# Optimization experiments

Measured on AMD Instinct MI355X. Metric: run time of the kernel, lower is better.

The kernel has to match this reference:

```python
import jax, jax.numpy as jnp
import numpy as np
from jax import lax

VOCAB = 128
UNITS = 1024
B, T = 64, 128


def setup_inputs() -> dict:
    key = jax.random.key(0)
    ks = jax.random.split(key, 8)
    tokens = jax.random.randint(ks[0], (B, T), 0, VOCAB)
    emb_table = jax.random.normal(ks[1], (VOCAB, UNITS), dtype=jnp.float32) * 0.05
    def dir_params(k):
        k1, k2, k3 = jax.random.split(k, 3)
        W = jax.random.normal(k1, (UNITS, 3 * UNITS), dtype=jnp.float32) * 0.02
        U = jax.random.normal(k2, (UNITS, 3 * UNITS), dtype=jnp.float32) * 0.02
        b = jnp.zeros((2, 3 * UNITS), dtype=jnp.float32)  # [input_bias, recurrent_bias] (reset_after=True)
        return W, U, b
    Wf, Uf, bf = dir_params(ks[2])
    Wb, Ub, bb = dir_params(ks[3])
    return {"tokens": tokens, "emb_table": emb_table,
            "Wf": Wf, "Uf": Uf, "bf": bf,
            "Wb": Wb, "Ub": Ub, "bb": bb}


def _gru_dir(emb, mask, W, U, b):
    """Masked GRU (Keras semantics, reset_after=True, gate order z,r,h).
    emb: [B,T,U] float, mask: [B,T] bool. Returns [B,T,U]."""
    units = W.shape[0]
    # Precompute input projection for all timesteps (one big GEMM).
    xp = jnp.einsum('btu,uv->btv', emb, W) + b[0]          # [B,T,3U]
    xp_t = jnp.transpose(xp, (1, 0, 2))                     # [T,B,3U]
    m_t = jnp.transpose(mask, (1, 0))                       # [T,B]
    h0 = jnp.zeros((emb.shape[0], units), dtype=emb.dtype)
    out0 = jnp.zeros_like(h0)

    def step(carry, inp):
        h, prev_out = carry
        x_t, mt = inp
        rec = h @ U + b[1]                                  # [B,3U]
        xz, xr, xh = jnp.split(x_t, 3, axis=-1)
        rz, rr, rh = jnp.split(rec, 3, axis=-1)
        z = jax.nn.sigmoid(xz + rz)
        r = jax.nn.sigmoid(xr + rr)
        hh = jnp.tanh(xh + r * rh)
        h_new = z * h + (1.0 - z) * hh
        m = mt[:, None]
        out = jnp.where(m, h_new, prev_out)  # masked steps copy previous output
        h_next = jnp.where(m, h_new, h)      # masked steps carry state
        return (h_next, out), out

    _, outs = lax.scan(step, (h0, out0), (xp_t, m_t))       # [T,B,U]
    return jnp.transpose(outs, (1, 0, 2))


def reference(tokens, emb_table, Wf, Uf, bf, Wb, Ub, bb):
    mask = tokens != 0                                      # mask_zero=True
    emb = emb_table[tokens]                                 # [B,T,U]
    fwd = _gru_dir(emb, mask, Wf, Uf, bf)
    # backward direction: reverse time, run GRU, reverse output back
    bwd = _gru_dir(emb[:, ::-1, :], mask[:, ::-1], Wb, Ub, bb)[:, ::-1, :]
    return fwd + bwd                                        # merge_mode='sum'
```

## Files before the change

### kernel.cpp

```cpp
#include <hip/hip_runtime.h>
#include <hip/hip_cooperative_groups.h>

namespace cg = cooperative_groups;

#define NWG 256
#define NT  256
#define B_  64
#define T_  128
#define U_  1024
#define C3  3072
#define SMEM_BYTES ((24*1024 + 2*64*12) * 4)

__device__ __forceinline__ float sigm(float x){ return 1.f/(1.f+__expf(-x)); }
__device__ __forceinline__ float tanh_(float x){ return 1.f - 2.f/(1.f+__expf(2.f*x)); }

__global__ void __launch_bounds__(NT, 1)
enc_kernel(const int* __restrict__ tok,
           const float* __restrict__ emb,
           const float* __restrict__ Wf, const float* __restrict__ Uf, const float* __restrict__ bfp,
           const float* __restrict__ Wb, const float* __restrict__ Ub, const float* __restrict__ bbp,
           float* __restrict__ out, float* __restrict__ ws)
{
  extern __shared__ float sm[];
  float* Ul   = sm;
  float* recl = sm + 24*1024;

  const int tid = threadIdx.x, wg = blockIdx.x;
  const int u0 = wg*4;

  float* xpv  = ws;
  float* embT = ws + 6144*128;
  float* hg   = ws + 6144*128 + 1024*128;

  cg::grid_group grid = cg::this_grid();
  const int gtid = wg*NT + tid;

  for (int i = gtid; i < 2*1024*64; i += NWG*NT) hg[i] = 0.f;
  for (int i = gtid; i < 128*1024; i += NWG*NT)
    embT[(i & 1023)*128 + (i >> 10)] = emb[i];

  #pragma unroll
  for (int i = 0; i < 24; ++i) {
    int flat = tid + i*NT;
    int k = flat / 6, rem = flat % 6;
    int dd = rem / 3, g = rem % 3;
    const float* M = dd ? Wb : Wf;
    float4 v4 = *(const float4*)&M[k*C3 + g*U_ + u0];
    Ul[(dd*12 + 0 + g)*1024 + k] = v4.x;
    Ul[(dd*12 + 3 + g)*1024 + k] = v4.y;
    Ul[(dd*12 + 6 + g)*1024 + k] = v4.z;
    Ul[(dd*12 + 9 + g)*1024 + k] = v4.w;
  }
  grid.sync();

  const int lane = tid & 63, wv = tid >> 6;
  const int d = wv >> 1, uu = wv & 1;
  const int bq = lane & 15, kq = lane >> 4;
  const float* ulds = Ul + (d*12 + uu*6)*1024;

  auto dot6 = [&](const float* src, int rs, float* r) {
    float acc[6][4];
    #pragma unroll
    for (int j=0;j<6;++j){acc[j][0]=acc[j][1]=acc[j][2]=acc[j][3]=0.f;}
    for (int kit = 0; kit < 64; ++kit) {
      float4 uv[6];
      #pragma unroll
      for (int j=0;j<6;++j) uv[j] = *(const float4*)(ulds + j*1024 + kq*256 + kit*4);
      #pragma unroll
      for (int kk=0;kk<4;++kk) {
        float4 h4 = *(const float4*)(src + (kit*4+kk)*rs);
        #pragma unroll
        for (int j=0;j<6;++j) {
          float w = kk==0?uv[j].x : kk==1?uv[j].y : kk==2?uv[j].z : uv[j].w;
          acc[j][0] += h4.x*w; acc[j][1] += h4.y*w;
          acc[j][2] += h4.z*w; acc[j][3] += h4.w*w;
        }
      }
    }
    #pragma unroll
    for (int j=0;j<6;++j){
      #pragma unroll
      for (int bi=0;bi<4;++bi){
        float v = acc[j][bi];
        v += __shfl_xor(v, 16, 64);
        v += __shfl_xor(v, 32, 64);
        acc[j][bi] = v;
      }
      r[j] = kq==0?acc[j][0] : kq==1?acc[j][1] : kq==2?acc[j][2] : acc[j][3];
    }
  };

  {
    const float* bias_d = d ? bbp : bfp;
    for (int half = 0; half < 2; ++half) {
      float r[6];
      dot6(embT + (kq*256)*128 + half*64 + bq*4, 128, r);
      int v = half*64 + bq*4 + kq;
      #pragma unroll
      for (int j=0;j<6;++j){
        int ul = j/3, g = j%3;
        int cp = g*U_ + u0 + uu*2 + ul;
        xpv[(d*C3 + cp)*128 + v] = r[j] + bias_d[cp];
      }
    }
  }
  __syncthreads();
  #pragma unroll
  for (int i = 0; i < 24; ++i) {
    int flat = tid + i*NT;
    int k = flat / 6, rem = flat % 6;
    int dd = rem / 3, g = rem % 3;
    const float* M = dd ? Ub : Uf;
    float4 v4 = *(const float4*)&M[k*C3 + g*U_ + u0];
    Ul[(dd*12 + 0 + g)*1024 + k] = v4.x;
    Ul[(dd*12 + 3 + g)*1024 + k] = v4.y;
    Ul[(dd*12 + 6 + g)*1024 + k] = v4.z;
    Ul[(dd*12 + 9 + g)*1024 + k] = v4.w;
  }
  __syncthreads();

  for (int s = 0; s < T_; ++s) {
    const float* hc = hg + (s&1)*(2*1024*64);
    float*       hn = hg + ((s+1)&1)*(2*1024*64);

    float r[6];
    dot6(hc + (d*1024 + kq*256)*64 + bq*4, 64, r);
    const int b = bq*4 + kq;
    #pragma unroll
    for (int j=0;j<6;++j) recl[(d*64 + b)*12 + uu*6 + j] = r[j];
    __syncthreads();

    {
      const int gd = tid >> 7, guu = (tid >> 6) & 1, gb = tid & 63;
      const int t = gd ? (T_-1 - s) : s;
      const int tk = tok[gb*T_ + t];
      const bool msk = (tk != 0);
      const float* bias = gd ? bbp : bfp;
      float o[2];
      #pragma unroll
      for (int ul=0; ul<2; ++ul) {
        const int u = u0 + guu*2 + ul;
        const int rb = (gd*64+gb)*12 + guu*6 + ul*3;
        float rz = recl[rb+0] + bias[C3 + u];
        float rr = recl[rb+1] + bias[C3 + U_ + u];
        float rh = recl[rb+2] + bias[C3 + 2*U_ + u];
        float xz = xpv[(gd*C3 +          u)*128 + tk];
        float xr = xpv[(gd*C3 +   U_  +  u)*128 + tk];
        float xh = xpv[(gd*C3 + 2*U_  +  u)*128 + tk];
        float hold = hc[(gd*1024 + u)*64 + gb];
        float z  = sigm(xz + rz);
        float rg = sigm(xr + rr);
        float th = tanh_(xh + rg*rh);
        float hnew = z*hold + (1.f - z)*th;
        float hx = msk ? hnew : hold;
        hn[(gd*1024 + u)*64 + gb] = hx;
        o[ul] = hx;
      }
      float2* op = (float2*)(out + (gb*T_ + t)*U_ + u0 + guu*2);
      if (s < 64) { *op = make_float2(o[0], o[1]); }
      else        { float2 pv = *op; *op = make_float2(pv.x + o[0], pv.y + o[1]); }
    }
    grid.sync();
  }
}

extern "C" void kernel_launch(void* const* d_in, const int* in_sizes, int n_in,
                              void* d_out, int out_size, void* d_ws, size_t ws_size,
                              hipStream_t stream) {
  const int*   tok = (const int*)  d_in[0];
  const float* emb = (const float*)d_in[1];
  const float* Wf  = (const float*)d_in[2];
  const float* Uf  = (const float*)d_in[3];
  const float* bfp = (const float*)d_in[4];
  const float* Wb  = (const float*)d_in[5];
  const float* Ub  = (const float*)d_in[6];
  const float* bbp = (const float*)d_in[7];
  float* outp = (float*)d_out;
  float* wsp  = (float*)d_ws;

  static bool attr_done = false;
  (void)attr_done;
  hipFuncSetAttribute((const void*)enc_kernel,
                      hipFuncAttributeMaxDynamicSharedMemorySize, SMEM_BYTES);

  void* args[] = { (void*)&tok, (void*)&emb, (void*)&Wf, (void*)&Uf, (void*)&bfp,
                   (void*)&Wb, (void*)&Ub, (void*)&bbp, (void*)&outp, (void*)&wsp };
  hipLaunchCooperativeKernel((const void*)enc_kernel, dim3(NWG), dim3(NT),
                             args, SMEM_BYTES, stream);
}
```

Measured before the change: 7.229 ms.

## Double threads per workgroup with K-split dot products and padded LDS layout

```diff
diff --git a/kernel.cpp b/kernel.cpp
--- a/kernel.cpp
+++ b/kernel.cpp
@@ -4,17 +4,22 @@
 namespace cg = cooperative_groups;
 
 #define NWG 256
-#define NT  256
+#define NT  512
 #define B_  64
 #define T_  128
 #define U_  1024
 #define C3  3072
-#define SMEM_BYTES ((24*1024 + 2*64*12) * 4)
+
+#define COLSTRIDE 1088
+#define U_LDS_FLOATS (24*COLSTRIDE)
+#define P_OFF   U_LDS_FLOATS
+#define REC_OFF (P_OFF + 6144)
+#define SMEM_BYTES ((U_LDS_FLOATS + 6144 + 1536)*4)
 
 __device__ __forceinline__ float sigm(float x){ return 1.f/(1.f+__expf(-x)); }
 __device__ __forceinline__ float tanh_(float x){ return 1.f - 2.f/(1.f+__expf(2.f*x)); }
 
-__global__ void __launch_bounds__(NT, 1)
+__global__ void __launch_bounds__(NT, 2)
 enc_kernel(const int* __restrict__ tok,
            const float* __restrict__ emb,
            const float* __restrict__ Wf, const float* __restrict__ Uf, const float* __restrict__ bfp,
@@ -23,7 +28,8 @@
 {
   extern __shared__ float sm[];
   float* Ul   = sm;
-  float* recl = sm + 24*1024;
+  float* Pl   = sm + P_OFF;
+  float* recl = sm + REC_OFF;
 
   const int tid = threadIdx.x, wg = blockIdx.x;
   const int u0 = wg*4;
@@ -39,38 +45,43 @@
   for (int i = gtid; i < 128*1024; i += NWG*NT)
     embT[(i & 1023)*128 + (i >> 10)] = emb[i];
 
-  #pragma unroll
-  for (int i = 0; i < 24; ++i) {
-    int flat = tid + i*NT;
-    int k = flat / 6, rem = flat % 6;
-    int dd = rem / 3, g = rem % 3;
-    const float* M = dd ? Wb : Wf;
-    float4 v4 = *(const float4*)&M[k*C3 + g*U_ + u0];
-    Ul[(dd*12 + 0 + g)*1024 + k] = v4.x;
-    Ul[(dd*12 + 3 + g)*1024 + k] = v4.y;
-    Ul[(dd*12 + 6 + g)*1024 + k] = v4.z;
-    Ul[(dd*12 + 9 + g)*1024 + k] = v4.w;
-  }
+  auto loadMat = [&](const float* Mf_, const float* Mb_) {
+    #pragma unroll
+    for (int i = 0; i < 12; ++i) {
+      int flat = tid + i*NT;
+      int k = flat / 6, rem = flat % 6;
+      int dd = rem / 3, g = rem % 3;
+      const float* M = dd ? Mb_ : Mf_;
+      float4 v4 = *(const float4*)&M[k*C3 + g*U_ + u0];
+      int koff = (k >> 6)*68 + (k & 63);
+      Ul[(dd*12 + 0*3 + g)*COLSTRIDE + koff] = v4.x;
+      Ul[(dd*12 + 1*3 + g)*COLSTRIDE + koff] = v4.y;
+      Ul[(dd*12 + 2*3 + g)*COLSTRIDE + koff] = v4.z;
+      Ul[(dd*12 + 3*3 + g)*COLSTRIDE + koff] = v4.w;
+    }
+  };
+
+  loadMat(Wf, Wb);
   grid.sync();
 
   const int lane = tid & 63, wv = tid >> 6;
-  const int d = wv >> 1, uu = wv & 1;
+  const int d = wv >> 2, kh = wv & 3;
   const int bq = lane & 15, kq = lane >> 4;
-  const float* ulds = Ul + (d*12 + uu*6)*1024;
+  const float* ubase = Ul + (d*12)*COLSTRIDE + (kh*4 + kq)*68;
 
-  auto dot6 = [&](const float* src, int rs, float* r) {
-    float acc[6][4];
+  auto dot12 = [&](const float* src, int rs, float* r) {
+    float acc[12][4];
     #pragma unroll
-    for (int j=0;j<6;++j){acc[j][0]=acc[j][1]=acc[j][2]=acc[j][3]=0.f;}
-    for (int kit = 0; kit < 64; ++kit) {
-      float4 uv[6];
+    for (int j=0;j<12;++j){acc[j][0]=acc[j][1]=acc[j][2]=acc[j][3]=0.f;}
+    for (int kit = 0; kit < 16; ++kit) {
+      float4 uv[12];
       #pragma unroll
-      for (int j=0;j<6;++j) uv[j] = *(const float4*)(ulds + j*1024 + kq*256 + kit*4);
+      for (int j=0;j<12;++j) uv[j] = *(const float4*)(ubase + j*COLSTRIDE + kit*4);
       #pragma unroll
       for (int kk=0;kk<4;++kk) {
         float4 h4 = *(const float4*)(src + (kit*4+kk)*rs);
         #pragma unroll
-        for (int j=0;j<6;++j) {
+        for (int j=0;j<12;++j) {
           float w = kk==0?uv[j].x : kk==1?uv[j].y : kk==2?uv[j].z : uv[j].w;
           acc[j][0] += h4.x*w; acc[j][1] += h4.y*w;
           acc[j][2] += h4.z*w; acc[j][3] += h4.w*w;
@@ -78,7 +89,7 @@
       }
     }
     #pragma unroll
-    for (int j=0;j<6;++j){
+    for (int j=0;j<12;++j){
       #pragma unroll
       for (int bi=0;bi<4;++bi){
         float v = acc[j][bi];
@@ -90,75 +101,71 @@
     }
   };
 
-  {
-    const float* bias_d = d ? bbp : bfp;
-    for (int half = 0; half < 2; ++half) {
-      float r[6];
-      dot6(embT + (kq*256)*128 + half*64 + bq*4, 128, r);
-      int v = half*64 + bq*4 + kq;
-      #pragma unroll
-      for (int j=0;j<6;++j){
-        int ul = j/3, g = j%3;
-        int cp = g*U_ + u0 + uu*2 + ul;
-        xpv[(d*C3 + cp)*128 + v] = r[j] + bias_d[cp];
-      }
+  for (int half = 0; half < 2; ++half) {
+    float r[12];
+    dot12(embT + (kh*256 + kq*64)*128 + half*64 + bq*4, 128, r);
+    const int vv = bq*4 + kq;
+    #pragma unroll
+    for (int j=0;j<12;++j) Pl[(d*12+j)*256 + kh*64 + vv] = r[j];
+    __syncthreads();
+    for (int e = tid; e < 1536; e += NT) {
+      int dc = e >> 6, v = e & 63;
+      float s_ = Pl[dc*256 + v] + Pl[dc*256 + 64 + v] + Pl[dc*256 + 128 + v] + Pl[dc*256 + 192 + v];
+      int dd = dc / 12, c = dc % 12;
+      int ul = c / 3, g = c % 3;
+      int cp = g*U_ + u0 + ul;
+      const float* brow = dd ? bbp : bfp;
+      xpv[(dd*C3 + cp)*128 + half*64 + v] = s_ + brow[cp];
     }
+    __syncthreads();
   }
+
+  loadMat(Uf, Ub);
   __syncthreads();
-  #pragma unroll
-  for (int i = 0; i < 24; ++i) {
-    int flat = tid + i*NT;
-    int k = flat / 6, rem = flat % 6;
-    int dd = rem / 3, g = rem % 3;
-    const float* M = dd ? Ub : Uf;
-    float4 v4 = *(const float4*)&M[k*C3 + g*U_ + u0];
-    Ul[(dd*12 + 0 + g)*1024 + k] = v4.x;
-    Ul[(dd*12 + 3 + g)*1024 + k] = v4.y;
-    Ul[(dd*12 + 6 + g)*1024 + k] = v4.z;
-    Ul[(dd*12 + 9 + g)*1024 + k] = v4.w;
-  }
-  __syncthreads();
+
+  const int gd = tid >> 8, grm = tid & 255, gb = grm >> 2, gul = grm & 3;
+  const int gu = u0 + gul;
+  const float* brow1 = (gd ? bbp : bfp) + C3;
+  const float bz1 = brow1[gu], br1 = brow1[U_ + gu], bh1 = brow1[2*U_ + gu];
 
   for (int s = 0; s < T_; ++s) {
     const float* hc = hg + (s&1)*(2*1024*64);
     float*       hn = hg + ((s+1)&1)*(2*1024*64);
 
-    float r[6];
-    dot6(hc + (d*1024 + kq*256)*64 + bq*4, 64, r);
+    float r[12];
+    dot12(hc + (d*1024 + kh*256 + kq*64)*64 + bq*4, 64, r);
     const int b = bq*4 + kq;
     #pragma unroll
-    for (int j=0;j<6;++j) recl[(d*64 + b)*12 + uu*6 + j] = r[j];
+    for (int j=0;j<12;++j) Pl[(d*12+j)*256 + kh*64 + b] = r[j];
+    __syncthreads();
+
+    #pragma unroll
+    for (int e = tid, it = 0; it < 3; ++it, e += NT) {
+      int dc = e >> 6, v = e & 63;
+      recl[e] = Pl[dc*256 + v] + Pl[dc*256 + 64 + v] + Pl[dc*256 + 128 + v] + Pl[dc*256 + 192 + v];
+    }
     __syncthreads();
 
     {
-      const int gd = tid >> 7, guu = (tid >> 6) & 1, gb = tid & 63;
       const int t = gd ? (T_-1 - s) : s;
       const int tk = tok[gb*T_ + t];
       const bool msk = (tk != 0);
-      const float* bias = gd ? bbp : bfp;
-      float o[2];
-      #pragma unroll
-      for (int ul=0; ul<2; ++ul) {
-        const int u = u0 + guu*2 + ul;
-        const int rb = (gd*64+gb)*12 + guu*6 + ul*3;
-        float rz = recl[rb+0] + bias[C3 + u];
-        float rr = recl[rb+1] + bias[C3 + U_ + u];
-        float rh = recl[rb+2] + bias[C3 + 2*U_ + u];
-        float xz = xpv[(gd*C3 +          u)*128 + tk];
-        float xr = xpv[(gd*C3 +   U_  +  u)*128 + tk];
-        float xh = xpv[(gd*C3 + 2*U_  +  u)*128 + tk];
-        float hold = hc[(gd*1024 + u)*64 + gb];
-        float z  = sigm(xz + rz);
-        float rg = sigm(xr + rr);
-        float th = tanh_(xh + rg*rh);
-        float hnew = z*hold + (1.f - z)*th;
-        float hx = msk ? hnew : hold;
-        hn[(gd*1024 + u)*64 + gb] = hx;
-        o[ul] = hx;
-      }
-      float2* op = (float2*)(out + (gb*T_ + t)*U_ + u0 + guu*2);
-      if (s < 64) { *op = make_float2(o[0], o[1]); }
-      else        { float2 pv = *op; *op = make_float2(pv.x + o[0], pv.y + o[1]); }
+      const int rb = (gd*12 + gul*3)*64 + gb;
+      float rz = recl[rb]        + bz1;
+      float rr = recl[rb + 64]   + br1;
+      float rh = recl[rb + 128]  + bh1;
+      float xz = xpv[(gd*C3 +          gu)*128 + tk];
+      float xr = xpv[(gd*C3 +   U_  +  gu)*128 + tk];
+      float xh = xpv[(gd*C3 + 2*U_  +  gu)*128 + tk];
+      float hold = hc[(gd*1024 + gu)*64 + gb];
+      float z  = sigm(xz + rz);
+      float rg = sigm(xr + rr);
+      float th = tanh_(xh + rg*rh);
+      float hnew = z*hold + (1.f - z)*th;
+      float hx = msk ? hnew : hold;
+      hn[(gd*1024 + gu)*64 + gb] = hx;
+      float* op = out + (gb*T_ + t)*U_ + gu;
+      if (s < 64) *op = hx; else *op += hx;
     }
     grid.sync();
   }
@@ -178,8 +185,6 @@
   float* outp = (float*)d_out;
   float* wsp  = (float*)d_ws;
 
-  static bool attr_done = false;
-  (void)attr_done;
   hipFuncSetAttribute((const void*)enc_kernel,
                       hipFuncAttributeMaxDynamicSharedMemorySize, SMEM_BYTES);
 
```

After: 5.922 ms. 18.1% less time.
